# Performance work log

Hardware: AMD Instinct MI355X
Metric: run time of the kernel (lower is better)

The kernel has to match this reference:

```python
import jax, jax.numpy as jnp
import numpy as np

B, S, H, NH = 4, 1024, 1024, 16
D = H // NH  # head dim = 64
MAXPOS = 1024
EPS = 1e-12


def setup_inputs() -> dict:
    key = jax.random.key(0)
    ks = jax.random.split(key, 12)
    sc = 0.02
    return {
        "hidden_states": jax.random.normal(ks[0], (B, S, H), jnp.float32),
        "attention_mask": jnp.zeros((B, 1, 1, S), jnp.float32),
        "Wq": jax.random.normal(ks[1], (H, H), jnp.float32) * sc,
        "bq": jnp.zeros((H,), jnp.float32),
        "Wk": jax.random.normal(ks[2], (H, H), jnp.float32) * sc,
        "bk": jnp.zeros((H,), jnp.float32),
        "Wv": jax.random.normal(ks[3], (H, H), jnp.float32) * sc,
        "bv": jnp.zeros((H,), jnp.float32),
        "dist_emb": jax.random.normal(ks[4], (2 * MAXPOS - 1, D), jnp.float32) * sc,
        "Wo": jax.random.normal(ks[5], (H, H), jnp.float32) * sc,
        "bo": jnp.zeros((H,), jnp.float32),
        "ln_g": jnp.ones((H,), jnp.float32),
        "ln_b": jnp.zeros((H,), jnp.float32),
    }


def _heads(x):  # [B,S,H] -> [B,NH,S,D]
    return x.reshape(B, S, NH, D).transpose(0, 2, 1, 3)


def reference(hidden_states, attention_mask, Wq, bq, Wk, bk, Wv, bv,
              dist_emb, Wo, bo, ln_g, ln_b):
    x = hidden_states
    q = _heads(x @ Wq.T + bq)  # [B,NH,S,D]
    k = _heads(x @ Wk.T + bk)
    v = _heads(x @ Wv.T + bv)

    scores = jnp.einsum("bhld,bhrd->bhlr", q, k)

    # relative_key_query positional bias
    pos = jnp.arange(S)
    distance = pos[:, None] - pos[None, :] + (MAXPOS - 1)  # [S,S]
    pe = dist_emb[distance]  # [S,S,D]
    scores = scores + jnp.einsum("bhld,lrd->bhlr", q, pe)
    scores = scores + jnp.einsum("bhrd,lrd->bhlr", k, pe)

    scores = scores / np.sqrt(D).astype(np.float32) + attention_mask
    probs = jax.nn.softmax(scores, axis=-1)  # dropout p=0 -> identity

    ctx = jnp.einsum("bhlr,bhrd->bhld", probs, v)
    ctx = ctx.transpose(0, 2, 1, 3).reshape(B, S, H)

    # BertSelfOutput: dense + residual + LayerNorm
    y = ctx @ Wo.T + bo + x
    mu = jnp.mean(y, axis=-1, keepdims=True)
    var = jnp.mean(jnp.square(y - mu), axis=-1, keepdims=True)
    return (y - mu) * jax.lax.rsqrt(var + EPS) * ln_g + ln_b
```

## Files before the change

kernel.cpp:

```cpp
#include <hip/hip_runtime.h>
#include <hip/hip_bf16.h>

#define BB 4
#define SS 1024
#define HH 1024
#define NHH 16
#define DD 64
#define MAXPOS 1024

typedef __hip_bfloat16 bf16;
typedef unsigned short ushort_t;
typedef __attribute__((ext_vector_type(8))) short short8;
typedef __attribute__((ext_vector_type(4))) float f32x4;
typedef __attribute__((ext_vector_type(4))) unsigned short us4;

#define MFMA_16x16x32(a, b, c) __builtin_amdgcn_mfma_f32_16x16x32_bf16((a), (b), (c), 0, 0, 0)

__device__ __forceinline__ float bu2f(ushort_t u) {
    union { unsigned int i; float f; } c; c.i = ((unsigned int)u) << 16; return c.f;
}
__device__ __forceinline__ ushort_t f2bu(float f) {
    __hip_bfloat16 h = __float2bfloat16(f);
    return *reinterpret_cast<ushort_t*>(&h);
}

__global__ void conv_all(const float* __restrict__ x,  const float* __restrict__ Wq,
                         const float* __restrict__ Wk, const float* __restrict__ Wv,
                         const float* __restrict__ Wo, const float* __restrict__ dist,
                         ushort_t* __restrict__ xb,  ushort_t* __restrict__ Wqb,
                         ushort_t* __restrict__ Wkb, ushort_t* __restrict__ Wvb,
                         ushort_t* __restrict__ Wob, ushort_t* __restrict__ Eb)
{
    const int i = blockIdx.x * 256 + threadIdx.x;
    const float* src; ushort_t* dst; int off;
    if (i < 1048576)      { src = x;  dst = xb;  off = i; }
    else if (i < 1310720) { src = Wq; dst = Wqb; off = i - 1048576; }
    else if (i < 1572864) { src = Wk; dst = Wkb; off = i - 1310720; }
    else if (i < 1835008) { src = Wv; dst = Wvb; off = i - 1572864; }
    else if (i < 2097152) { src = Wo; dst = Wob; off = i - 1835008; }
    else if (i < 2129920) {
        const int j = i - 2097152;
        float4 f = (j < 32752) ? ((const float4*)dist)[j] : make_float4(0.f, 0.f, 0.f, 0.f);
        us4 u;
        u[0] = f2bu(f.x); u[1] = f2bu(f.y); u[2] = f2bu(f.z); u[3] = f2bu(f.w);
        ((us4*)Eb)[j] = u;
        return;
    } else return;
    float4 f = ((const float4*)src)[off];
    us4 u;
    u[0] = f2bu(f.x); u[1] = f2bu(f.y); u[2] = f2bu(f.z); u[3] = f2bu(f.w);
    ((us4*)dst)[off] = u;
}

__global__ __launch_bounds__(256)
void qkv_mfma(const ushort_t* __restrict__ xb,
              const ushort_t* __restrict__ Wqb, const float* __restrict__ bq,
              const ushort_t* __restrict__ Wkb, const float* __restrict__ bk,
              const ushort_t* __restrict__ Wvb, const float* __restrict__ bv,
              ushort_t* __restrict__ q, ushort_t* __restrict__ k,
              ushort_t* __restrict__ vt)
{
    const int which = blockIdx.z;
    const ushort_t* __restrict__ W    = (which == 0) ? Wqb : (which == 1) ? Wkb : Wvb;
    const float*    __restrict__ bias = (which == 0) ? bq  : (which == 1) ? bk  : bv;

    const int tid = threadIdx.x, w = tid >> 6, lane = tid & 63;
    const int quad = lane >> 4, lq = lane & 15;
    const int wm = w >> 1, wn = w & 1;
    const int m0 = blockIdx.y * 128 + wm * 64;
    const int n0 = blockIdx.x * 128 + wn * 64;

    f32x4 acc[4][4];
#pragma unroll
    for (int i = 0; i < 4; i++)
#pragma unroll
        for (int j = 0; j < 4; j++) acc[i][j] = (f32x4){0.f, 0.f, 0.f, 0.f};

    const ushort_t* aB = xb + (size_t)(m0 + lq) * 1024 + quad * 8;
    const ushort_t* bB = W  + (size_t)(n0 + lq) * 1024 + quad * 8;

#pragma unroll 2
    for (int k0 = 0; k0 < 1024; k0 += 32) {
        short8 af[4], bf[4];
#pragma unroll
        for (int i = 0; i < 4; i++) af[i] = *(const short8*)(aB + i * 16 * 1024 + k0);
#pragma unroll
        for (int j = 0; j < 4; j++) bf[j] = *(const short8*)(bB + j * 16 * 1024 + k0);
#pragma unroll
        for (int i = 0; i < 4; i++)
#pragma unroll
            for (int j = 0; j < 4; j++)
                acc[i][j] = MFMA_16x16x32(af[i], bf[j], acc[i][j]);
    }

    if (which == 2) {
#pragma unroll
        for (int j = 0; j < 4; j++) {
            const int n  = n0 + j * 16 + lq;
            const int h_ = n >> 6, d_ = n & 63;
            const float bb = bias[n];
#pragma unroll
            for (int i = 0; i < 4; i++) {
                const int m  = m0 + i * 16 + quad * 4;
                const int b_ = m >> 10, l = m & 1023;
                us4 pv;
#pragma unroll
                for (int g = 0; g < 4; g++) pv[g] = f2bu(acc[i][j][g] + bb);
                *(us4*)(vt + (((size_t)(b_ * NHH) + h_) * DD + d_) * SS + l) = pv;
            }
        }
    } else {
        ushort_t* __restrict__ out = (which == 0) ? q : k;
        const float sc = (which == 0) ? 0.125f : 1.0f;
#pragma unroll
        for (int j = 0; j < 4; j++) {
            const int n  = n0 + j * 16 + lq;
            const int h_ = n >> 6, d_ = n & 63;
            const float bb = bias[n];
#pragma unroll
            for (int i = 0; i < 4; i++) {
#pragma unroll
                for (int g = 0; g < 4; g++) {
                    const int m  = m0 + i * 16 + quad * 4 + g;
                    const int b_ = m >> 10, l = m & 1023;
                    out[(((size_t)(b_ * NHH) + h_) * SS + l) * DD + d_] =
                        f2bu((acc[i][j][g] + bb) * sc);
                }
            }
        }
    }
}

__global__ __launch_bounds__(256)
void attn_mfma(const ushort_t* __restrict__ qb, const ushort_t* __restrict__ kb,
               const ushort_t* __restrict__ vt, const ushort_t* __restrict__ Eb,
               const float* __restrict__ mask, ushort_t* __restrict__ ctx)
{
    const int l0 = blockIdx.x * 64;
    const int h  = blockIdx.y, b = blockIdx.z;
    const int tid  = threadIdx.x;
    const int w    = tid >> 6;
    const int lane = tid & 63;
    const int quad = lane >> 4, lq = lane & 15;

    __shared__ __align__(16) ushort_t QEsT[128 * 68];
    __shared__ __align__(16) ushort_t KEsT[128 * 68];
    __shared__ __align__(16) ushort_t PsT [64 * 72];

    const ushort_t* qbh = qb + (size_t)(b * NHH + h) * SS * DD;
    const ushort_t* kbh = kb + (size_t)(b * NHH + h) * SS * DD;
    const ushort_t* vth = vt + (size_t)(b * NHH + h) * DD * SS;

    short8 qa0, qa1;
    {
        const ushort_t* p = qbh + (l0 + w * 16 + lq) * DD + quad * 8;
        qa0 = *(const short8*)p;
        qa1 = *(const short8*)(p + 32);
    }
    const int l_loc = w * 16 + lq;

    f32x4 Oacc[4];
#pragma unroll
    for (int dt = 0; dt < 4; dt++) Oacc[dt] = (f32x4){0.f, 0.f, 0.f, 0.f};
    float mrow = -3e38f, lrow = 0.f;

    for (int rt = 0; rt < 16; rt++) {
        const int r0   = rt * 64;
        const int dmin = l0 - r0 + 960;

        short8 kf0[4], kf1[4];
#pragma unroll
        for (int ct = 0; ct < 4; ct++) {
            const ushort_t* p = kbh + (r0 + ct * 16 + lq) * DD + quad * 8;
            kf0[ct] = *(const short8*)p;
            kf1[ct] = *(const short8*)(p + 32);
        }
        float mk[4];
#pragma unroll
        for (int g = 0; g < 4; g++) mk[g] = mask[b * SS + r0 + w * 16 + quad * 4 + g];

        __syncthreads();

#pragma unroll
        for (int tt = 0; tt < 8; tt++) {
            const ushort_t* ep = Eb + (size_t)(dmin + tt * 16 + lq) * DD + quad * 8;
            short8 e0 = *(const short8*)ep;
            short8 e1 = *(const short8*)(ep + 32);
            f32x4 qe = (f32x4){0.f, 0.f, 0.f, 0.f};
            f32x4 ke = (f32x4){0.f, 0.f, 0.f, 0.f};
            qe = MFMA_16x16x32(qa0, e0, qe);
            qe = MFMA_16x16x32(qa1, e1, qe);
            ke = MFMA_16x16x32(kf0[w], e0, ke);
            ke = MFMA_16x16x32(kf1[w], e1, ke);
            us4 pq, pk;
#pragma unroll
            for (int g = 0; g < 4; g++) {
                pq[g] = f2bu(qe[g]);
                pk[g] = f2bu(ke[g] * 0.125f + mk[g]);
            }
            const int trow = tt * 16 + lq;
            *(us4*)&QEsT[trow * 68 + w * 16 + quad * 4] = pq;
            *(us4*)&KEsT[trow * 68 + w * 16 + quad * 4] = pk;
        }

        f32x4 st[4];
#pragma unroll
        for (int ct = 0; ct < 4; ct++) {
            f32x4 a = (f32x4){0.f, 0.f, 0.f, 0.f};
            a = MFMA_16x16x32(kf0[ct], qa0, a);
            a = MFMA_16x16x32(kf1[ct], qa1, a);
            st[ct] = a;
        }

        __syncthreads();

        float p[4][4];
        float tmax = -3e38f;
#pragma unroll
        for (int ct = 0; ct < 4; ct++) {
#pragma unroll
            for (int g = 0; g < 4; g++) {
                const int r_loc = ct * 16 + quad * 4 + g;
                const int t = l_loc - r_loc + 63;
                float s = st[ct][g] + bu2f(QEsT[t * 68 + l_loc])
                                    + bu2f(KEsT[t * 68 + r_loc]);
                p[ct][g] = s;
                tmax = fmaxf(tmax, s);
            }
        }
        tmax = fmaxf(tmax, __shfl_xor(tmax, 16));
        tmax = fmaxf(tmax, __shfl_xor(tmax, 32));
        const float mnew  = fmaxf(mrow, tmax);
        const float alpha = __expf(mrow - mnew);
        mrow = mnew;
        float psum = 0.f;
#pragma unroll
        for (int ct = 0; ct < 4; ct++)
#pragma unroll
            for (int g = 0; g < 4; g++) {
                const float e = __expf(p[ct][g] - mrow);
                p[ct][g] = e;
                psum += e;
            }
        psum += __shfl_xor(psum, 16);
        psum += __shfl_xor(psum, 32);
        lrow = lrow * alpha + psum;
#pragma unroll
        for (int dt = 0; dt < 4; dt++)
#pragma unroll
            for (int g = 0; g < 4; g++) Oacc[dt][g] *= alpha;

#pragma unroll
        for (int ct = 0; ct < 4; ct++) {
            us4 pp;
#pragma unroll
            for (int g = 0; g < 4; g++) pp[g] = f2bu(p[ct][g]);
            *(us4*)&PsT[l_loc * 72 + ct * 16 + quad * 4] = pp;
        }

#pragma unroll
        for (int c = 0; c < 2; c++) {
            short8 pb = *(const short8*)&PsT[l_loc * 72 + c * 32 + quad * 8];
#pragma unroll
            for (int dt = 0; dt < 4; dt++) {
                const ushort_t* vp = vth + (size_t)(dt * 16 + lq) * SS
                                         + r0 + c * 32 + quad * 8;
                short8 va = *(const short8*)vp;
                Oacc[dt] = MFMA_16x16x32(va, pb, Oacc[dt]);
            }
        }
    }

    const float invl = 1.0f / lrow;
    ushort_t* cbase = ctx + (size_t)(b * SS + l0 + w * 16 + lq) * HH + h * DD;
#pragma unroll
    for (int dt = 0; dt < 4; dt++) {
        us4 po;
#pragma unroll
        for (int g = 0; g < 4; g++) po[g] = f2bu(Oacc[dt][g] * invl);
        *(us4*)(cbase + dt * 16 + quad * 4) = po;
    }
}

__global__ __launch_bounds__(256)
void out_proj(const ushort_t* __restrict__ ctx, const ushort_t* __restrict__ Wob,
              const float* __restrict__ bo, const float* __restrict__ x,
              float* __restrict__ y)
{
    const int tid = threadIdx.x, w = tid >> 6, lane = tid & 63;
    const int quad = lane >> 4, lq = lane & 15;
    const int wm = w >> 1, wn = w & 1;
    const int m0 = blockIdx.y * 128 + wm * 64;
    const int n0 = blockIdx.x * 64 + wn * 32;

    f32x4 acc[4][2];
#pragma unroll
    for (int i = 0; i < 4; i++)
#pragma unroll
        for (int j = 0; j < 2; j++) acc[i][j] = (f32x4){0.f, 0.f, 0.f, 0.f};

    const ushort_t* aB = ctx + (size_t)(m0 + lq) * 1024 + quad * 8;
    const ushort_t* bB = Wob + (size_t)(n0 + lq) * 1024 + quad * 8;

#pragma unroll 2
    for (int k0 = 0; k0 < 1024; k0 += 32) {
        short8 af[4], bf[2];
#pragma unroll
        for (int i = 0; i < 4; i++) af[i] = *(const short8*)(aB + i * 16 * 1024 + k0);
#pragma unroll
        for (int j = 0; j < 2; j++) bf[j] = *(const short8*)(bB + j * 16 * 1024 + k0);
#pragma unroll
        for (int i = 0; i < 4; i++)
#pragma unroll
            for (int j = 0; j < 2; j++)
                acc[i][j] = MFMA_16x16x32(af[i], bf[j], acc[i][j]);
    }

#pragma unroll
    for (int j = 0; j < 2; j++) {
        const int n = n0 + j * 16 + lq;
        const float bb = bo[n];
#pragma unroll
        for (int i = 0; i < 4; i++) {
#pragma unroll
            for (int g = 0; g < 4; g++) {
                const int m = m0 + i * 16 + quad * 4 + g;
                y[(size_t)m * 1024 + n] = acc[i][j][g] + bb + x[(size_t)m * 1024 + n];
            }
        }
    }
}

__global__ void layernorm(const float* __restrict__ y, const float* __restrict__ g,
                          const float* __restrict__ beta, float* __restrict__ out)
{
    const int row = blockIdx.x;
    const int tid = threadIdx.x;

    __shared__ float red[256];
    __shared__ float red2[256];

    const float4 t4 = *(const float4*)(y + (size_t)row * 1024 + tid * 4);
    float s  = t4.x + t4.y + t4.z + t4.w;
    float s2 = t4.x * t4.x + t4.y * t4.y + t4.z * t4.z + t4.w * t4.w;
    red[tid] = s;
    red2[tid] = s2;
    __syncthreads();
    for (int st = 128; st > 0; st >>= 1) {
        if (tid < st) { red[tid] += red[tid + st]; red2[tid] += red2[tid + st]; }
        __syncthreads();
    }
    const float mu  = red[0] * (1.0f / 1024.0f);
    const float var = red2[0] * (1.0f / 1024.0f) - mu * mu;
    const float rs  = rsqrtf(var + 1e-12f);

    const float4 g4 = *(const float4*)(g + tid * 4);
    const float4 b4 = *(const float4*)(beta + tid * 4);
    float4 o;
    o.x = (t4.x - mu) * rs * g4.x + b4.x;
    o.y = (t4.y - mu) * rs * g4.y + b4.y;
    o.z = (t4.z - mu) * rs * g4.z + b4.z;
    o.w = (t4.w - mu) * rs * g4.w + b4.w;
    *(float4*)(out + (size_t)row * 1024 + tid * 4) = o;
}

extern "C" void kernel_launch(void* const* d_in, const int* in_sizes, int n_in,
                              void* d_out, int out_size, void* d_ws, size_t ws_size,
                              hipStream_t stream)
{
    const float* x    = (const float*)d_in[0];
    const float* mask = (const float*)d_in[1];
    const float* Wq   = (const float*)d_in[2];
    const float* bq   = (const float*)d_in[3];
    const float* Wk   = (const float*)d_in[4];
    const float* bk   = (const float*)d_in[5];
    const float* Wv   = (const float*)d_in[6];
    const float* bv   = (const float*)d_in[7];
    const float* dist = (const float*)d_in[8];
    const float* Wo   = (const float*)d_in[9];
    const float* bo   = (const float*)d_in[10];
    const float* g    = (const float*)d_in[11];
    const float* be   = (const float*)d_in[12];

    char* wsb = (char*)d_ws;
    ushort_t* xb  = (ushort_t*)(wsb);
    ushort_t* Wqb = (ushort_t*)(wsb + ( 8u << 20));
    ushort_t* Wkb = (ushort_t*)(wsb + (10u << 20));
    ushort_t* Wvb = (ushort_t*)(wsb + (12u << 20));
    ushort_t* Wob = (ushort_t*)(wsb + (14u << 20));
    ushort_t* qbu = (ushort_t*)(wsb + (16u << 20));
    ushort_t* kbu = (ushort_t*)(wsb + (24u << 20));
    ushort_t* vtb = (ushort_t*)(wsb + (32u << 20));
    ushort_t* Eb  = (ushort_t*)(wsb + (40u << 20));
    float*    y   = (float*)(wsb + (16u << 20));
    ushort_t* ctxb = (ushort_t*)d_out;

    conv_all<<<8320, 256, 0, stream>>>(x, Wq, Wk, Wv, Wo, dist,
                                       xb, Wqb, Wkb, Wvb, Wob, Eb);
    qkv_mfma<<<dim3(8, 32, 3), 256, 0, stream>>>(xb, Wqb, bq, Wkb, bk, Wvb, bv,
                                                 qbu, kbu, vtb);
    attn_mfma<<<dim3(16, 16, 4), 256, 0, stream>>>(qbu, kbu, vtb, Eb, mask, ctxb);
    out_proj<<<dim3(16, 32), 256, 0, stream>>>(ctxb, Wob, bo, x, y);
    layernorm<<<4096, 256, 0, stream>>>(y, g, be, (float*)d_out);
}
```

Before: 484.0 us.

## Stage GEMM tiles into LDS via direct global-to-LDS loads

The QKV and output-projection GEMMs now copy each 128x32 A and B tile into shared memory with global_load_lds, then read MFMA fragments from LDS. Before, every wave loaded its fragments straight from global memory, so the two waves sharing a row or column both fetched the same data. The output projection tile also grows to 128x128, halving its grid. The loop is single-buffered with two barriers per k-step, so load latency is not overlapped with compute and the 64-byte LDS row stride may cause bank conflicts.

```diff
diff --git a/kernel.cpp b/kernel.cpp
--- a/kernel.cpp
+++ b/kernel.cpp
@@ -22,6 +22,12 @@
 __device__ __forceinline__ ushort_t f2bu(float f) {
     __hip_bfloat16 h = __float2bfloat16(f);
     return *reinterpret_cast<ushort_t*>(&h);
+}
+__device__ __forceinline__ void stage16(const ushort_t* g, ushort_t* l) {
+    __builtin_amdgcn_global_load_lds(
+        (const __attribute__((address_space(1))) void*)g,
+        (__attribute__((address_space(3))) void*)l,
+        16, 0, 0);
 }
 
 __global__ void conv_all(const float* __restrict__ x,  const float* __restrict__ Wq,
@@ -67,8 +73,13 @@
     const int tid = threadIdx.x, w = tid >> 6, lane = tid & 63;
     const int quad = lane >> 4, lq = lane & 15;
     const int wm = w >> 1, wn = w & 1;
-    const int m0 = blockIdx.y * 128 + wm * 64;
-    const int n0 = blockIdx.x * 128 + wn * 64;
+    const int bm = blockIdx.y * 128;
+    const int bn = blockIdx.x * 128;
+    const int m0 = bm + wm * 64;
+    const int n0 = bn + wn * 64;
+
+    __shared__ __align__(16) ushort_t As[128 * 32];
+    __shared__ __align__(16) ushort_t Bs[128 * 32];
 
     f32x4 acc[4][4];
 #pragma unroll
@@ -76,16 +87,32 @@
 #pragma unroll
         for (int j = 0; j < 4; j++) acc[i][j] = (f32x4){0.f, 0.f, 0.f, 0.f};
 
-    const ushort_t* aB = xb + (size_t)(m0 + lq) * 1024 + quad * 8;
-    const ushort_t* bB = W  + (size_t)(n0 + lq) * 1024 + quad * 8;
-
-#pragma unroll 2
+    const int lrow = lane >> 2;
+    const int lcol = (lane & 3) * 8;
+    const ushort_t* aS0 = xb + (size_t)(bm + w * 16 + lrow) * 1024 + lcol;
+    const ushort_t* aS1 = aS0 + 64 * 1024;
+    const ushort_t* bS0 = W  + (size_t)(bn + w * 16 + lrow) * 1024 + lcol;
+    const ushort_t* bS1 = bS0 + 64 * 1024;
+    ushort_t* const aD0 = As + w * 512;
+    ushort_t* const aD1 = As + (w + 4) * 512;
+    ushort_t* const bD0 = Bs + w * 512;
+    ushort_t* const bD1 = Bs + (w + 4) * 512;
+
     for (int k0 = 0; k0 < 1024; k0 += 32) {
+        __syncthreads();
+        stage16(aS0 + k0, aD0);
+        stage16(aS1 + k0, aD1);
+        stage16(bS0 + k0, bD0);
+        stage16(bS1 + k0, bD1);
+        __syncthreads();
+
         short8 af[4], bf[4];
 #pragma unroll
-        for (int i = 0; i < 4; i++) af[i] = *(const short8*)(aB + i * 16 * 1024 + k0);
-#pragma unroll
-        for (int j = 0; j < 4; j++) bf[j] = *(const short8*)(bB + j * 16 * 1024 + k0);
+        for (int i = 0; i < 4; i++)
+            af[i] = *(const short8*)&As[(wm * 64 + i * 16 + lq) * 32 + quad * 8];
+#pragma unroll
+        for (int j = 0; j < 4; j++)
+            bf[j] = *(const short8*)&Bs[(wn * 64 + j * 16 + lq) * 32 + quad * 8];
 #pragma unroll
         for (int i = 0; i < 4; i++)
 #pragma unroll
@@ -290,34 +317,55 @@
     const int tid = threadIdx.x, w = tid >> 6, lane = tid & 63;
     const int quad = lane >> 4, lq = lane & 15;
     const int wm = w >> 1, wn = w & 1;
-    const int m0 = blockIdx.y * 128 + wm * 64;
-    const int n0 = blockIdx.x * 64 + wn * 32;
-
-    f32x4 acc[4][2];
+    const int bm = blockIdx.y * 128;
+    const int bn = blockIdx.x * 128;
+    const int m0 = bm + wm * 64;
+    const int n0 = bn + wn * 64;
+
+    __shared__ __align__(16) ushort_t As[128 * 32];
+    __shared__ __align__(16) ushort_t Bs[128 * 32];
+
+    f32x4 acc[4][4];
 #pragma unroll
     for (int i = 0; i < 4; i++)
 #pragma unroll
-        for (int j = 0; j < 2; j++) acc[i][j] = (f32x4){0.f, 0.f, 0.f, 0.f};
-
-    const ushort_t* aB = ctx + (size_t)(m0 + lq) * 1024 + quad * 8;
-    const ushort_t* bB = Wob + (size_t)(n0 + lq) * 1024 + quad * 8;
-
-#pragma unroll 2
+        for (int j = 0; j < 4; j++) acc[i][j] = (f32x4){0.f, 0.f, 0.f, 0.f};
+
+    const int lrow = lane >> 2;
+    const int lcol = (lane & 3) * 8;
+    const ushort_t* aS0 = ctx + (size_t)(bm + w * 16 + lrow) * 1024 + lcol;
+    const ushort_t* aS1 = aS0 + 64 * 1024;
+    const ushort_t* bS0 = Wob + (size_t)(bn + w * 16 + lrow) * 1024 + lcol;
+    const ushort_t* bS1 = bS0 + 64 * 1024;
+    ushort_t* const aD0 = As + w * 512;
+    ushort_t* const aD1 = As + (w + 4) * 512;
+    ushort_t* const bD0 = Bs + w * 512;
+    ushort_t* const bD1 = Bs + (w + 4) * 512;
+
     for (int k0 = 0; k0 < 1024; k0 += 32) {
-        short8 af[4], bf[2];
-#pragma unroll
-        for (int i = 0; i < 4; i++) af[i] = *(const short8*)(aB + i * 16 * 1024 + k0);
-#pragma unroll
-        for (int j = 0; j < 2; j++) bf[j] = *(const short8*)(bB + j * 16 * 1024 + k0);
+        __syncthreads();
+        stage16(aS0 + k0, aD0);
+        stage16(aS1 + k0, aD1);
+        stage16(bS0 + k0, bD0);
+        stage16(bS1 + k0, bD1);
+        __syncthreads();
+
+        short8 af[4], bf[4];
 #pragma unroll
         for (int i = 0; i < 4; i++)
-#pragma unroll
-            for (int j = 0; j < 2; j++)
+            af[i] = *(const short8*)&As[(wm * 64 + i * 16 + lq) * 32 + quad * 8];
+#pragma unroll
+        for (int j = 0; j < 4; j++)
+            bf[j] = *(const short8*)&Bs[(wn * 64 + j * 16 + lq) * 32 + quad * 8];
+#pragma unroll
+        for (int i = 0; i < 4; i++)
+#pragma unroll
+            for (int j = 0; j < 4; j++)
                 acc[i][j] = MFMA_16x16x32(af[i], bf[j], acc[i][j]);
     }
 
 #pragma unroll
-    for (int j = 0; j < 2; j++) {
+    for (int j = 0; j < 4; j++) {
         const int n = n0 + j * 16 + lq;
         const float bb = bo[n];
 #pragma unroll
@@ -400,6 +448,6 @@
     qkv_mfma<<<dim3(8, 32, 3), 256, 0, stream>>>(xb, Wqb, bq, Wkb, bk, Wvb, bv,
                                                  qbu, kbu, vtb);
     attn_mfma<<<dim3(16, 16, 4), 256, 0, stream>>>(qbu, kbu, vtb, Eb, mask, ctxb);
-    out_proj<<<dim3(16, 32), 256, 0, stream>>>(ctxb, Wob, bo, x, y);
+    out_proj<<<dim3(8, 32), 256, 0, stream>>>(ctxb, Wob, bo, x, y);
     layernorm<<<4096, 256, 0, stream>>>(y, g, be, (float*)d_out);
 }
```

Measured after the change: 414.3 us (median of 2 runs). 14.4% less time.
